# Kernel optimization log

Measured on AMD Instinct MI355X. Metric: run time of the kernel, lower is better.

The kernel has to match this reference:

```python
import jax, jax.numpy as jnp
import numpy as np

D_MODEL, H, D_K = 768, 12, 64
B, S = 2, 2048
NEG = -1.0e9


def setup_inputs() -> dict:
    key = jax.random.key(0)
    ks = jax.random.split(key, 7)
    q = jax.random.normal(ks[0], (B, S, D_MODEL), dtype=jnp.float32)
    k = jax.random.normal(ks[1], (B, S, D_MODEL), dtype=jnp.float32)
    v = jax.random.normal(ks[2], (B, S, D_MODEL), dtype=jnp.float32)
    mask = jnp.tril(jnp.ones((S, S), dtype=jnp.int32))[None, None]  # [1,1,S,S] causal
    sc = 1.0 / np.sqrt(D_MODEL)
    w_q = jax.random.normal(ks[3], (D_MODEL, D_MODEL), dtype=jnp.float32) * sc
    w_k = jax.random.normal(ks[4], (D_MODEL, D_MODEL), dtype=jnp.float32) * sc
    w_v = jax.random.normal(ks[5], (D_MODEL, D_MODEL), dtype=jnp.float32) * sc
    w_o = jax.random.normal(ks[6], (D_MODEL, D_MODEL), dtype=jnp.float32) * sc
    return {"q": q, "k": k, "v": v, "mask": mask,
            "w_q": w_q, "w_k": w_k, "w_v": w_v, "w_o": w_o}


def reference(q, k, v, mask, w_q, w_k, w_v, w_o):
    # nn.Linear(x) = x @ W.T ; split heads: [B,S,D] -> [B,H,S,Dk]
    def split_heads(x, w):
        y = jnp.einsum('bsd,ed->bse', x, w)
        return y.reshape(x.shape[0], x.shape[1], H, D_K).transpose(0, 2, 1, 3)

    qh = split_heads(q, w_q)
    kh = split_heads(k, w_k)
    vh = split_heads(v, w_v)
    scores = jnp.einsum('bhqd,bhkd->bhqk', qh, kh) / jnp.sqrt(jnp.float32(D_K))
    scores = jnp.where(mask == 0, jnp.float32(NEG), scores)
    attn = jax.nn.softmax(scores, axis=-1)  # dropout p=0 -> identity
    ctx = jnp.einsum('bhqk,bhkd->bhqd', attn, vh)
    ctx = ctx.transpose(0, 2, 1, 3).reshape(q.shape[0], q.shape[1], D_MODEL)
    return jnp.einsum('bsd,ed->bse', ctx, w_o)
```

## Files before the change

### kernel.cpp

```cpp
#include <hip/hip_runtime.h>

#define DM   768
#define HN   12
#define DKH  64
#define BSZ  2
#define SEQ  2048
#define MROWS (BSZ*SEQ)
#define NEGBIG -1.0e9f
#define NSLOT 40
#define QSCALE 0.18033688011112042f

typedef __bf16 bf16;
typedef __bf16 bf16x8 __attribute__((ext_vector_type(8)));
typedef __bf16 bf16x4 __attribute__((ext_vector_type(4)));
typedef float  f32x4  __attribute__((ext_vector_type(4)));
typedef unsigned int uint32;

__device__ __forceinline__ void gload_lds16(const void* g, void* l) {
    __builtin_amdgcn_global_load_lds(
        (const __attribute__((address_space(1))) char*)g,
        (__attribute__((address_space(3))) char*)l, 16, 0, 0);
}

__global__ __launch_bounds__(256) void gemm_qkv(
    const float* __restrict__ xq, const float* __restrict__ xk, const float* __restrict__ xv,
    const float* __restrict__ wq, const float* __restrict__ wk, const float* __restrict__ wv,
    bf16* __restrict__ qh, bf16* __restrict__ kh, bf16* __restrict__ vt)
{
    __shared__ float Asf[128 * 32];
    __shared__ float Bsf[128 * 32];

    const float* A; const float* Bw; bf16* Out; float qs;
    if      (blockIdx.z == 0) { A = xq; Bw = wq; Out = qh; qs = QSCALE; }
    else if (blockIdx.z == 1) { A = xk; Bw = wk; Out = kh; qs = 1.0f; }
    else                      { A = xv; Bw = wv; Out = vt; qs = 1.0f; }
    const bool vout = (blockIdx.z == 2);

    const int t = threadIdx.x, w = t >> 6, lane = t & 63;
    const int g = lane >> 4, lo = lane & 15;
    const int mt = blockIdx.x * 128, nt = blockIdx.y * 128;
    const int wr = (w >> 1) * 64, wc = (w & 1) * 64;

    f32x4 acc[4][4] = {};

    for (int k0 = 0; k0 < DM; k0 += 32) {
        #pragma unroll
        for (int i = 0; i < 4; i++) {
            int c = i * 256 + t;
            int row = c >> 3, cc = (c & 7) ^ (row & 7);
            gload_lds16(A  + (size_t)(mt + row) * DM + k0 + cc * 4, (char*)Asf + c * 16);
            gload_lds16(Bw + (size_t)(nt + row) * DM + k0 + cc * 4, (char*)Bsf + c * 16);
        }
        asm volatile("s_waitcnt vmcnt(0)" ::: "memory");
        __syncthreads();

        bf16x8 af[4], bfr[4];
        #pragma unroll
        for (int m = 0; m < 4; m++) {
            const char* rp = (const char*)Asf + (wr + m * 16 + lo) * 128;
            float4 f0 = *(const float4*)(rp + (((2 * g)     ^ (lo & 7)) << 4));
            float4 f1 = *(const float4*)(rp + (((2 * g + 1) ^ (lo & 7)) << 4));
            bf16x8 a;
            a[0] = (bf16)f0.x; a[1] = (bf16)f0.y; a[2] = (bf16)f0.z; a[3] = (bf16)f0.w;
            a[4] = (bf16)f1.x; a[5] = (bf16)f1.y; a[6] = (bf16)f1.z; a[7] = (bf16)f1.w;
            af[m] = a;
        }
        #pragma unroll
        for (int n = 0; n < 4; n++) {
            const char* rp = (const char*)Bsf + (wc + n * 16 + lo) * 128;
            float4 f0 = *(const float4*)(rp + (((2 * g)     ^ (lo & 7)) << 4));
            float4 f1 = *(const float4*)(rp + (((2 * g + 1) ^ (lo & 7)) << 4));
            bf16x8 b;
            b[0] = (bf16)f0.x; b[1] = (bf16)f0.y; b[2] = (bf16)f0.z; b[3] = (bf16)f0.w;
            b[4] = (bf16)f1.x; b[5] = (bf16)f1.y; b[6] = (bf16)f1.z; b[7] = (bf16)f1.w;
            bfr[n] = b;
        }
        #pragma unroll
        for (int m = 0; m < 4; m++)
            #pragma unroll
            for (int n = 0; n < 4; n++)
                acc[m][n] = __builtin_amdgcn_mfma_f32_16x16x32_bf16(af[m], bfr[n], acc[m][n], 0, 0, 0);
        __syncthreads();
    }

    if (!vout) {
        #pragma unroll
        for (int m = 0; m < 4; m++) {
            #pragma unroll
            for (int n = 0; n < 4; n++) {
                #pragma unroll
                for (int r = 0; r < 4; r++) {
                    int gm = mt + wr + m * 16 + g * 4 + r;
                    int gn = nt + wc + n * 16 + lo;
                    int b = gm >> 11, s = gm & 2047, h = gn >> 6, d = gn & 63;
                    Out[(((size_t)b * HN + h) * SEQ + s) * DKH + d] = (bf16)(acc[m][n][r] * qs);
                }
            }
        }
    } else {
        #pragma unroll
        for (int m = 0; m < 4; m++) {
            #pragma unroll
            for (int n = 0; n < 4; n++) {
                int gm = mt + wr + m * 16 + g * 4;
                int gn = nt + wc + n * 16 + lo;
                int b = gm >> 11, s0 = gm & 2047, h = gn >> 6, d = gn & 63;
                bf16x4 pk;
                #pragma unroll
                for (int r = 0; r < 4; r++) pk[r] = (bf16)acc[m][n][r];
                *(bf16x4*)&Out[(((size_t)b * HN + h) * DKH + d) * SEQ + s0] = pk;
            }
        }
    }
}

__global__ __launch_bounds__(256) void gemm_out(
    const bf16* __restrict__ Actx, const float* __restrict__ Bw, float* __restrict__ Out)
{
    __shared__ bf16  As[128 * 32];
    __shared__ float Bsf[128 * 32];

    const int t = threadIdx.x, w = t >> 6, lane = t & 63;
    const int g = lane >> 4, lo = lane & 15;
    const int mt = blockIdx.x * 128, nt = blockIdx.y * 128;
    const int wr = (w >> 1) * 64, wc = (w & 1) * 64;

    f32x4 acc[4][4] = {};

    for (int k0 = 0; k0 < DM; k0 += 32) {
        #pragma unroll
        for (int i = 0; i < 2; i++) {
            int c = i * 256 + t;
            int row = c >> 2, col = (c & 3) * 8;
            gload_lds16(Actx + (size_t)(mt + row) * DM + k0 + col, (char*)As + c * 16);
        }
        #pragma unroll
        for (int i = 0; i < 4; i++) {
            int c = i * 256 + t;
            int row = c >> 3, cc = (c & 7) ^ (row & 7);
            gload_lds16(Bw + (size_t)(nt + row) * DM + k0 + cc * 4, (char*)Bsf + c * 16);
        }
        asm volatile("s_waitcnt vmcnt(0)" ::: "memory");
        __syncthreads();

        bf16x8 af[4], bfr[4];
        #pragma unroll
        for (int m = 0; m < 4; m++)
            af[m] = *(const bf16x8*)&As[(wr + m * 16 + lo) * 32 + g * 8];
        #pragma unroll
        for (int n = 0; n < 4; n++) {
            const char* rp = (const char*)Bsf + (wc + n * 16 + lo) * 128;
            float4 f0 = *(const float4*)(rp + (((2 * g)     ^ (lo & 7)) << 4));
            float4 f1 = *(const float4*)(rp + (((2 * g + 1) ^ (lo & 7)) << 4));
            bf16x8 b;
            b[0] = (bf16)f0.x; b[1] = (bf16)f0.y; b[2] = (bf16)f0.z; b[3] = (bf16)f0.w;
            b[4] = (bf16)f1.x; b[5] = (bf16)f1.y; b[6] = (bf16)f1.z; b[7] = (bf16)f1.w;
            bfr[n] = b;
        }
        #pragma unroll
        for (int m = 0; m < 4; m++)
            #pragma unroll
            for (int n = 0; n < 4; n++)
                acc[m][n] = __builtin_amdgcn_mfma_f32_16x16x32_bf16(af[m], bfr[n], acc[m][n], 0, 0, 0);
        __syncthreads();
    }

    #pragma unroll
    for (int m = 0; m < 4; m++) {
        #pragma unroll
        for (int n = 0; n < 4; n++) {
            #pragma unroll
            for (int r = 0; r < 4; r++) {
                int gm = mt + wr + m * 16 + g * 4 + r;
                int gn = nt + wc + n * 16 + lo;
                Out[(size_t)gm * DM + gn] = acc[m][n][r];
            }
        }
    }
}

__global__ __launch_bounds__(256, 3) void flash_split(
    const bf16* __restrict__ qh, const bf16* __restrict__ kh,
    const bf16* __restrict__ vt, bf16* __restrict__ ctx,
    bf16* __restrict__ pO, float* __restrict__ pM, float* __restrict__ pL)
{
    __shared__ bf16 Ks[2][4096];
    __shared__ bf16 Vs[2][4096];
    __shared__ bf16 pl[4][1024];

    const int bid = blockIdx.x;
    const int slot = bid / 24;
    const int bh = bid % 24;

    int qt, p, np;
    if (slot < 16)      { qt = 15 - (slot >> 2); p = slot & 3;  np = 4; }
    else if (slot < 28) { int s = slot - 16; qt = 11 - s / 3; p = s % 3; np = 3; }
    else if (slot < 36) { int s = slot - 28; qt = 7 - (s >> 1); p = s & 1; np = 2; }
    else                { qt = 39 - slot; p = 0; np = 1; }

    const int T = 2 * qt + 2;
    const int bse = T / np, rem = T - bse * np;
    const int cnt   = bse + (p < rem ? 1 : 0);
    const int start = p * bse + (p < rem ? p : rem);

    const int qb = qt * 128;
    const int t = threadIdx.x, w = t >> 6, lane = t & 63;
    const int g = lane >> 4, lo = lane & 15;
    const size_t base = (size_t)bh * SEQ * DKH;
    const char* khead = (const char*)(kh + base);
    const char* vhead = (const char*)(vt + base);

    uint32 koff[2], voff[2];
    #pragma unroll
    for (int i = 0; i < 2; i++) {
        int c = w * 128 + i * 64 + lane;
        int r = c >> 3, s = c & 7;
        int sw = s ^ (r & 7);
        koff[i] = (uint32)(r * 128  + 16 * sw);
        voff[i] = (uint32)(r * 4096 + 16 * sw);
    }
    const uint32 kr0 = (uint32)(128 * lo + 16 * (g ^ (lo & 7)));
    const uint32 kr1 = kr0 ^ 64;

    uint32 pw[4], pr[2];
    #pragma unroll
    for (int cg = 0; cg < 4; cg++)
        pw[cg] = (uint32)(lo * 128 + (((2 * cg + (g >> 1)) ^ (lo & 7)) << 4) + (g & 1) * 8);
    #pragma unroll
    for (int kq = 0; kq < 2; kq++)
        pr[kq] = (uint32)(lo * 128 + (((4 * kq + g) ^ (lo & 7)) << 4));
    char* plb = (char*)&pl[w][0];

    const int qrow0 = qb + 16 * w + lo;
    const int qrow1 = qb + 64 + 16 * w + lo;
    const bf16* qp0 = qh + base + (size_t)qrow0 * DKH + g * 8;
    const bf16* qp1 = qh + base + (size_t)qrow1 * DKH + g * 8;
    bf16x8 qa0 = *(const bf16x8*)qp0;
    bf16x8 qa1 = *(const bf16x8*)(qp0 + 32);
    bf16x8 qb0 = *(const bf16x8*)qp1;
    bf16x8 qb1 = *(const bf16x8*)(qp1 + 32);

    f32x4 O0[4] = {}, O1[4] = {};
    float m0 = -1e30f, l0 = 0.0f, m1 = -1e30f, l1 = 0.0f;

    #pragma unroll
    for (int i = 0; i < 2; i++) {
        int c16 = (w * 128 + i * 64 + lane) * 16;
        gload_lds16(khead + (size_t)start * 8192 + koff[i], (char*)&Ks[0][0] + c16);
        gload_lds16(vhead + (size_t)start * 128  + voff[i], (char*)&Vs[0][0] + c16);
    }
    asm volatile("s_waitcnt vmcnt(0)" ::: "memory");
    __syncthreads();

    for (int it = 0; it < cnt; ++it) {
        const int kt = start + it;
        const int par = it & 1, nxt = par ^ 1;
        if (it + 1 < cnt) {
            const char* ks = khead + (size_t)(kt + 1) * 8192;
            const char* vs = vhead + (size_t)(kt + 1) * 128;
            #pragma unroll
            for (int i = 0; i < 2; i++) {
                int c16 = (w * 128 + i * 64 + lane) * 16;
                gload_lds16(ks + koff[i], (char*)&Ks[nxt][0] + c16);
                gload_lds16(vs + voff[i], (char*)&Vs[nxt][0] + c16);
            }
        }

        const bool act0  = (kt != T - 1);
        const bool diag0 = (kt == T - 2);
        const bool diag1 = (kt == T - 1);

        const char* Kp = (const char*)&Ks[par][0];
        f32x4 s0[4], s1[4];
        {
            bf16x8 kf0[4], kf1[4];
            #pragma unroll
            for (int cg = 0; cg < 4; cg++) {
                kf0[cg] = *(const bf16x8*)(Kp + cg * 2048 + kr0);
                kf1[cg] = *(const bf16x8*)(Kp + cg * 2048 + kr1);
            }
            __builtin_amdgcn_s_setprio(1);
            if (act0) {
                #pragma unroll
                for (int cg = 0; cg < 4; cg++) {
                    f32x4 z = {0.0f, 0.0f, 0.0f, 0.0f};
                    z = __builtin_amdgcn_mfma_f32_16x16x32_bf16(kf0[cg], qa0, z, 0, 0, 0);
                    z = __builtin_amdgcn_mfma_f32_16x16x32_bf16(kf1[cg], qa1, z, 0, 0, 0);
                    s0[cg] = z;
                }
            }
            #pragma unroll
            for (int cg = 0; cg < 4; cg++) {
                f32x4 z = {0.0f, 0.0f, 0.0f, 0.0f};
                z = __builtin_amdgcn_mfma_f32_16x16x32_bf16(kf0[cg], qb0, z, 0, 0, 0);
                z = __builtin_amdgcn_mfma_f32_16x16x32_bf16(kf1[cg], qb1, z, 0, 0, 0);
                s1[cg] = z;
            }
            __builtin_amdgcn_s_setprio(0);
        }

        if (act0 && diag0) {
            #pragma unroll
            for (int cg = 0; cg < 4; cg++)
                #pragma unroll
                for (int r = 0; r < 4; r++) {
                    int ki = kt * 64 + cg * 16 + 4 * g + r;
                    s0[cg][r] = (ki > qrow0) ? NEGBIG : s0[cg][r];
                }
        }
        if (diag1) {
            #pragma unroll
            for (int cg = 0; cg < 4; cg++)
                #pragma unroll
                for (int r = 0; r < 4; r++) {
                    int ki = kt * 64 + cg * 16 + 4 * g + r;
                    s1[cg][r] = (ki > qrow1) ? NEGBIG : s1[cg][r];
                }
        }

        if (act0) {
            float mx = fmaxf(fmaxf(fmaxf(s0[0][0], s0[0][1]), fmaxf(s0[0][2], s0[0][3])),
                             fmaxf(fmaxf(s0[1][0], s0[1][1]), fmaxf(s0[1][2], s0[1][3])));
            mx = fmaxf(mx, fmaxf(fmaxf(fmaxf(s0[2][0], s0[2][1]), fmaxf(s0[2][2], s0[2][3])),
                                 fmaxf(fmaxf(s0[3][0], s0[3][1]), fmaxf(s0[3][2], s0[3][3]))));
            mx = fmaxf(mx, __shfl_xor(mx, 16, 64));
            mx = fmaxf(mx, __shfl_xor(mx, 32, 64));
            if (!__all(mx - m0 <= 8.0f)) {
                float mnew = fmaxf(m0, mx);
                float scl = __builtin_exp2f(m0 - mnew);
                m0 = mnew; l0 *= scl;
                float s4[4];
                #pragma unroll
                for (int r = 0; r < 4; r++) s4[r] = __shfl(scl, 4 * g + r, 64);
                #pragma unroll
                for (int dg = 0; dg < 4; dg++)
                    #pragma unroll
                    for (int r = 0; r < 4; r++) O0[dg][r] *= s4[r];
            }
            float rs = 0.0f;
            #pragma unroll
            for (int cg = 0; cg < 4; cg++)
                #pragma unroll
                for (int r = 0; r < 4; r++) {
                    s0[cg][r] = __builtin_exp2f(s0[cg][r] - m0);
                    rs += s0[cg][r];
                }
            rs += __shfl_xor(rs, 16, 64);
            rs += __shfl_xor(rs, 32, 64);
            l0 += rs;
        }
        {
            float mx = fmaxf(fmaxf(fmaxf(s1[0][0], s1[0][1]), fmaxf(s1[0][2], s1[0][3])),
                             fmaxf(fmaxf(s1[1][0], s1[1][1]), fmaxf(s1[1][2], s1[1][3])));
            mx = fmaxf(mx, fmaxf(fmaxf(fmaxf(s1[2][0], s1[2][1]), fmaxf(s1[2][2], s1[2][3])),
                                 fmaxf(fmaxf(s1[3][0], s1[3][1]), fmaxf(s1[3][2], s1[3][3]))));
            mx = fmaxf(mx, __shfl_xor(mx, 16, 64));
            mx = fmaxf(mx, __shfl_xor(mx, 32, 64));
            if (!__all(mx - m1 <= 8.0f)) {
                float mnew = fmaxf(m1, mx);
                float scl = __builtin_exp2f(m1 - mnew);
                m1 = mnew; l1 *= scl;
                float s4[4];
                #pragma unroll
                for (int r = 0; r < 4; r++) s4[r] = __shfl(scl, 4 * g + r, 64);
                #pragma unroll
                for (int dg = 0; dg < 4; dg++)
                    #pragma unroll
                    for (int r = 0; r < 4; r++) O1[dg][r] *= s4[r];
            }
            float rs = 0.0f;
            #pragma unroll
            for (int cg = 0; cg < 4; cg++)
                #pragma unroll
                for (int r = 0; r < 4; r++) {
                    s1[cg][r] = __builtin_exp2f(s1[cg][r] - m1);
                    rs += s1[cg][r];
                }
            rs += __shfl_xor(rs, 16, 64);
            rs += __shfl_xor(rs, 32, 64);
            l1 += rs;
        }

        const char* Vp = (const char*)&Vs[par][0];
        bf16x8 vv[8];
        #pragma unroll
        for (int kq = 0; kq < 2; kq++)
            #pragma unroll
            for (int dblk = 0; dblk < 4; dblk++)
                vv[kq * 4 + dblk] = *(const bf16x8*)
                    (Vp + (dblk * 16 + lo) * 128 + 16 * ((4 * kq + g) ^ (lo & 7)));

        if (act0) {
            #pragma unroll
            for (int cg = 0; cg < 4; cg++) {
                bf16x4 pk;
                #pragma unroll
                for (int r = 0; r < 4; r++) pk[r] = (bf16)s0[cg][r];
                *(bf16x4*)(plb + pw[cg]) = pk;
            }
        }
        asm volatile("s_waitcnt lgkmcnt(0)" ::: "memory");
        __builtin_amdgcn_sched_barrier(0);
        if (act0) {
            __builtin_amdgcn_s_setprio(1);
            #pragma unroll
            for (int kq = 0; kq < 2; kq++) {
                bf16x8 pa = *(const bf16x8*)(plb + pr[kq]);
                #pragma unroll
                for (int dblk = 0; dblk < 4; dblk++)
                    O0[dblk] = __builtin_amdgcn_mfma_f32_16x16x32_bf16(pa, vv[kq * 4 + dblk], O0[dblk], 0, 0, 0);
            }
            __builtin_amdgcn_s_setprio(0);
        }
        __builtin_amdgcn_sched_barrier(0);
        {
            #pragma unroll
            for (int cg = 0; cg < 4; cg++) {
                bf16x4 pk;
                #pragma unroll
                for (int r = 0; r < 4; r++) pk[r] = (bf16)s1[cg][r];
                *(bf16x4*)(plb + pw[cg]) = pk;
            }
            asm volatile("s_waitcnt lgkmcnt(0)" ::: "memory");
            __builtin_amdgcn_sched_barrier(0);
            __builtin_amdgcn_s_setprio(1);
            #pragma unroll
            for (int kq = 0; kq < 2; kq++) {
                bf16x8 pa = *(const bf16x8*)(plb + pr[kq]);
                #pragma unroll
                for (int dblk = 0; dblk < 4; dblk++)
                    O1[dblk] = __builtin_amdgcn_mfma_f32_16x16x32_bf16(pa, vv[kq * 4 + dblk], O1[dblk], 0, 0, 0);
            }
            __builtin_amdgcn_s_setprio(0);
        }

        asm volatile("s_waitcnt vmcnt(0)" ::: "memory");
        __syncthreads();
    }

    if (np == 1) {
        const int b = bh / HN, h = bh % HN;
        float inv0[4], inv1[4];
        #pragma unroll
        for (int r = 0; r < 4; r++) {
            inv0[r] = 1.0f / __shfl(l0, 4 * g + r, 64);
            inv1[r] = 1.0f / __shfl(l1, 4 * g + r, 64);
        }
        #pragma unroll
        for (int dg = 0; dg < 4; dg++) {
            #pragma unroll
            for (int r = 0; r < 4; r++) {
                int row0 = qb + 16 * w + g * 4 + r;
                int row1 = qb + 64 + 16 * w + g * 4 + r;
                ctx[((size_t)(b * SEQ + row0)) * DM + h * DKH + dg * 16 + lo] =
                    (bf16)(O0[dg][r] * inv0[r]);
                ctx[((size_t)(b * SEQ + row1)) * DM + h * DKH + dg * 16 + lo] =
                    (bf16)(O1[dg][r] * inv1[r]);
            }
        }
    } else {
        const int pslot = bh * NSLOT + slot;
        bf16* po = pO + (size_t)pslot * 128 * 64;
        #pragma unroll
        for (int dg = 0; dg < 4; dg++) {
            #pragma unroll
            for (int r = 0; r < 4; r++) {
                int r0 = 16 * w + 4 * g + r;
                po[r0 * 64 + dg * 16 + lo]        = (bf16)O0[dg][r];
                po[(64 + r0) * 64 + dg * 16 + lo] = (bf16)O1[dg][r];
            }
        }
        if (g == 0) {
            pM[pslot * 128 + 16 * w + lo]      = m0;
            pL[pslot * 128 + 16 * w + lo]      = l0;
            pM[pslot * 128 + 64 + 16 * w + lo] = m1;
            pL[pslot * 128 + 64 + 16 * w + lo] = l1;
        }
    }
}

__global__ __launch_bounds__(256) void flash_combine(
    const bf16* __restrict__ pO, const float* __restrict__ pM,
    const float* __restrict__ pL, bf16* __restrict__ ctx)
{
    const int bh = blockIdx.x;
    const int qt = 4 + blockIdx.y;
    int np, s0;
    if (qt >= 12)     { np = 4; s0 = (15 - qt) * 4; }
    else if (qt >= 8) { np = 3; s0 = 16 + (11 - qt) * 3; }
    else              { np = 2; s0 = 28 + (7 - qt) * 2; }

    const int t = threadIdx.x;
    const int row = t >> 1, dh = (t & 1) * 32;
    const int pbase = bh * NSLOT + s0;

    float mi[4], wi[4];
    float mstar = -1e30f;
    #pragma unroll
    for (int i = 0; i < 4; i++)
        if (i < np) { mi[i] = pM[(pbase + i) * 128 + row]; mstar = fmaxf(mstar, mi[i]); }
    float lsum = 0.0f;
    #pragma unroll
    for (int i = 0; i < 4; i++)
        if (i < np) { wi[i] = __builtin_exp2f(mi[i] - mstar); lsum += wi[i] * pL[(pbase + i) * 128 + row]; }
    const float linv = 1.0f / lsum;

    const int b = bh / HN, h = bh % HN;
    bf16* crow = ctx + ((size_t)(b * SEQ + qt * 128 + row)) * DM + h * DKH + dh;

    #pragma unroll
    for (int d0 = 0; d0 < 32; d0 += 8) {
        float acc[8] = {};
        #pragma unroll
        for (int i = 0; i < 4; i++) {
            if (i < np) {
                bf16x8 o = *(const bf16x8*)&pO[((size_t)(pbase + i) * 128 + row) * 64 + dh + d0];
                #pragma unroll
                for (int j = 0; j < 8; j++) acc[j] += wi[i] * (float)o[j];
            }
        }
        bf16x8 ov;
        #pragma unroll
        for (int j = 0; j < 8; j++) ov[j] = (bf16)(acc[j] * linv);
        *(bf16x8*)(crow + d0) = ov;
    }
}

extern "C" void kernel_launch(void* const* d_in, const int* in_sizes, int n_in,
                              void* d_out, int out_size, void* d_ws, size_t ws_size,
                              hipStream_t stream) {
    const float* q  = (const float*)d_in[0];
    const float* k  = (const float*)d_in[1];
    const float* v  = (const float*)d_in[2];
    const float* wq = (const float*)d_in[4];
    const float* wk = (const float*)d_in[5];
    const float* wv = (const float*)d_in[6];
    const float* wo = (const float*)d_in[7];
    float* out = (float*)d_out;

    const size_t NX = (size_t)MROWS * DM;

    bf16* p = (bf16*)d_ws;
    bf16* qhp = p; p += NX;
    bf16* khp = p; p += NX;
    bf16* vtp = p; p += NX;
    bf16* ctxp = p; p += NX;
    bf16* pO = p; p += (size_t)24 * NSLOT * 128 * 64;
    float* pM = (float*)p;
    float* pL = pM + 24 * NSLOT * 128;

    gemm_qkv<<<dim3(MROWS / 128, DM / 128, 3), 256, 0, stream>>>(
        q, k, v, wq, wk, wv, qhp, khp, vtp);

    flash_split<<<24 * NSLOT, 256, 0, stream>>>(qhp, khp, vtp, ctxp, pO, pM, pL);
    flash_combine<<<dim3(24, 12), 256, 0, stream>>>(pO, pM, pL, ctxp);

    gemm_out<<<dim3(MROWS / 128, DM / 128), 256, 0, stream>>>(ctxp, wo, out);
}
```

Measured before the change: 116.3 us.

## Pre-convert QKV inputs to bf16 and double-buffer QKV GEMM; split P buffers in attention

Adds a conversion kernel that turns the fp32 activations and Q/K/V weights into bf16 in workspace. The QKV GEMM then loads bf16 tiles with BK=64 into double-buffered LDS, prefetching the next tile while computing the current one, so the per-tile fp32-to-bf16 conversion in the inner loop goes away. In flash_split, the P tiles for both row groups get separate LDS halves, which lets both be written right after softmax and both PV MFMA groups run back-to-back without an intermediate wait. The cost is an extra kernel launch plus a full read and write of the fp32 inputs, more LDS per block, and reuse of the bf16 input buffers as the split-partial workspace.

```diff
diff --git a/kernel.cpp b/kernel.cpp
--- a/kernel.cpp
+++ b/kernel.cpp
@@ -22,15 +22,39 @@
         (__attribute__((address_space(3))) char*)l, 16, 0, 0);
 }
 
+__global__ __launch_bounds__(256) void cvt6(
+    const float* __restrict__ a, const float* __restrict__ b, const float* __restrict__ c,
+    const float* __restrict__ d3, const float* __restrict__ e, const float* __restrict__ f,
+    bf16* __restrict__ x, bf16* __restrict__ y, bf16* __restrict__ z,
+    bf16* __restrict__ u, bf16* __restrict__ v, bf16* __restrict__ wbuf,
+    int nx, int nw)
+{
+    const float* s; bf16* d; int n;
+    switch (blockIdx.y) {
+        case 0: s = a;  d = x;    n = nx; break;
+        case 1: s = b;  d = y;    n = nx; break;
+        case 2: s = c;  d = z;    n = nx; break;
+        case 3: s = d3; d = u;    n = nw; break;
+        case 4: s = e;  d = v;    n = nw; break;
+        default: s = f; d = wbuf; n = nw; break;
+    }
+    int i = (blockIdx.x * 256 + threadIdx.x) * 4;
+    if (i + 3 < n) {
+        float4 vv = *(const float4*)(s + i);
+        bf16x4 o; o[0] = (bf16)vv.x; o[1] = (bf16)vv.y; o[2] = (bf16)vv.z; o[3] = (bf16)vv.w;
+        *(bf16x4*)(d + i) = o;
+    }
+}
+
 __global__ __launch_bounds__(256) void gemm_qkv(
-    const float* __restrict__ xq, const float* __restrict__ xk, const float* __restrict__ xv,
-    const float* __restrict__ wq, const float* __restrict__ wk, const float* __restrict__ wv,
+    const bf16* __restrict__ xq, const bf16* __restrict__ xk, const bf16* __restrict__ xv,
+    const bf16* __restrict__ wq, const bf16* __restrict__ wk, const bf16* __restrict__ wv,
     bf16* __restrict__ qh, bf16* __restrict__ kh, bf16* __restrict__ vt)
 {
-    __shared__ float Asf[128 * 32];
-    __shared__ float Bsf[128 * 32];
-
-    const float* A; const float* Bw; bf16* Out; float qs;
+    __shared__ bf16 As[2][128 * 64];
+    __shared__ bf16 Bs[2][128 * 64];
+
+    const bf16* A; const bf16* Bw; bf16* Out; float qs;
     if      (blockIdx.z == 0) { A = xq; Bw = wq; Out = qh; qs = QSCALE; }
     else if (blockIdx.z == 1) { A = xk; Bw = wk; Out = kh; qs = 1.0f; }
     else                      { A = xv; Bw = wv; Out = vt; qs = 1.0f; }
@@ -42,13 +66,118 @@
     const int wr = (w >> 1) * 64, wc = (w & 1) * 64;
 
     f32x4 acc[4][4] = {};
+    const int NT = DM / 64;
+
+    uint32 soff[4];
+    #pragma unroll
+    for (int i = 0; i < 4; i++) {
+        int c = i * 256 + t;
+        int row = c >> 3, s = c & 7;
+        soff[i] = (uint32)(row * DM + (s ^ (row & 7)) * 8);
+    }
+
+    #pragma unroll
+    for (int i = 0; i < 4; i++) {
+        int c16 = (i * 256 + t) * 16;
+        gload_lds16(A  + (size_t)mt * DM + soff[i], (char*)&As[0][0] + c16);
+        gload_lds16(Bw + (size_t)nt * DM + soff[i], (char*)&Bs[0][0] + c16);
+    }
+    asm volatile("s_waitcnt vmcnt(0)" ::: "memory");
+    __syncthreads();
+
+    for (int it = 0; it < NT; ++it) {
+        const int par = it & 1, nxt = par ^ 1;
+        if (it + 1 < NT) {
+            const size_t k0 = (size_t)(it + 1) * 64;
+            #pragma unroll
+            for (int i = 0; i < 4; i++) {
+                int c16 = (i * 256 + t) * 16;
+                gload_lds16(A  + (size_t)mt * DM + k0 + soff[i], (char*)&As[nxt][0] + c16);
+                gload_lds16(Bw + (size_t)nt * DM + k0 + soff[i], (char*)&Bs[nxt][0] + c16);
+            }
+        }
+
+        const char* Ap = (const char*)&As[par][0];
+        const char* Bp = (const char*)&Bs[par][0];
+        #pragma unroll
+        for (int h = 0; h < 2; h++) {
+            bf16x8 af[4], bfr[4];
+            #pragma unroll
+            for (int m = 0; m < 4; m++) {
+                int row = wr + m * 16 + lo;
+                af[m] = *(const bf16x8*)(Ap + row * 128 + 16 * ((4 * h + g) ^ (lo & 7)));
+            }
+            #pragma unroll
+            for (int n = 0; n < 4; n++) {
+                int row = wc + n * 16 + lo;
+                bfr[n] = *(const bf16x8*)(Bp + row * 128 + 16 * ((4 * h + g) ^ (lo & 7)));
+            }
+            #pragma unroll
+            for (int m = 0; m < 4; m++)
+                #pragma unroll
+                for (int n = 0; n < 4; n++)
+                    acc[m][n] = __builtin_amdgcn_mfma_f32_16x16x32_bf16(af[m], bfr[n], acc[m][n], 0, 0, 0);
+        }
+
+        asm volatile("s_waitcnt vmcnt(0)" ::: "memory");
+        __syncthreads();
+    }
+
+    if (!vout) {
+        #pragma unroll
+        for (int m = 0; m < 4; m++) {
+            #pragma unroll
+            for (int n = 0; n < 4; n++) {
+                #pragma unroll
+                for (int r = 0; r < 4; r++) {
+                    int gm = mt + wr + m * 16 + g * 4 + r;
+                    int gn = nt + wc + n * 16 + lo;
+                    int b = gm >> 11, s = gm & 2047, h = gn >> 6, d = gn & 63;
+                    Out[(((size_t)b * HN + h) * SEQ + s) * DKH + d] = (bf16)(acc[m][n][r] * qs);
+                }
+            }
+        }
+    } else {
+        #pragma unroll
+        for (int m = 0; m < 4; m++) {
+            #pragma unroll
+            for (int n = 0; n < 4; n++) {
+                int gm = mt + wr + m * 16 + g * 4;
+                int gn = nt + wc + n * 16 + lo;
+                int b = gm >> 11, s0 = gm & 2047, h = gn >> 6, d = gn & 63;
+                bf16x4 pk;
+                #pragma unroll
+                for (int r = 0; r < 4; r++) pk[r] = (bf16)acc[m][n][r];
+                *(bf16x4*)&Out[(((size_t)b * HN + h) * DKH + d) * SEQ + s0] = pk;
+            }
+        }
+    }
+}
+
+__global__ __launch_bounds__(256) void gemm_out(
+    const bf16* __restrict__ Actx, const float* __restrict__ Bw, float* __restrict__ Out)
+{
+    __shared__ bf16  As[128 * 32];
+    __shared__ float Bsf[128 * 32];
+
+    const int t = threadIdx.x, w = t >> 6, lane = t & 63;
+    const int g = lane >> 4, lo = lane & 15;
+    const int mt = blockIdx.x * 128, nt = blockIdx.y * 128;
+    const int wr = (w >> 1) * 64, wc = (w & 1) * 64;
+
+    f32x4 acc[4][4] = {};
 
     for (int k0 = 0; k0 < DM; k0 += 32) {
+        #pragma unroll
+        for (int i = 0; i < 2; i++) {
+            int c = i * 256 + t;
+            int row = c >> 2, col = (c & 3) * 8;
+            gload_lds16(Actx + (size_t)(mt + row) * DM + k0 + col, (char*)As + c * 16);
+        }
         #pragma unroll
         for (int i = 0; i < 4; i++) {
             int c = i * 256 + t;
             int row = c >> 3, cc = (c & 7) ^ (row & 7);
-            gload_lds16(A  + (size_t)(mt + row) * DM + k0 + cc * 4, (char*)Asf + c * 16);
             gload_lds16(Bw + (size_t)(nt + row) * DM + k0 + cc * 4, (char*)Bsf + c * 16);
         }
         asm volatile("s_waitcnt vmcnt(0)" ::: "memory");
@@ -56,15 +185,8 @@
 
         bf16x8 af[4], bfr[4];
         #pragma unroll
-        for (int m = 0; m < 4; m++) {
-            const char* rp = (const char*)Asf + (wr + m * 16 + lo) * 128;
-            float4 f0 = *(const float4*)(rp + (((2 * g)     ^ (lo & 7)) << 4));
-            float4 f1 = *(const float4*)(rp + (((2 * g + 1) ^ (lo & 7)) << 4));
-            bf16x8 a;
-            a[0] = (bf16)f0.x; a[1] = (bf16)f0.y; a[2] = (bf16)f0.z; a[3] = (bf16)f0.w;
-            a[4] = (bf16)f1.x; a[5] = (bf16)f1.y; a[6] = (bf16)f1.z; a[7] = (bf16)f1.w;
-            af[m] = a;
-        }
+        for (int m = 0; m < 4; m++)
+            af[m] = *(const bf16x8*)&As[(wr + m * 16 + lo) * 32 + g * 8];
         #pragma unroll
         for (int n = 0; n < 4; n++) {
             const char* rp = (const char*)Bsf + (wc + n * 16 + lo) * 128;
@@ -83,88 +205,6 @@
         __syncthreads();
     }
 
-    if (!vout) {
-        #pragma unroll
-        for (int m = 0; m < 4; m++) {
-            #pragma unroll
-            for (int n = 0; n < 4; n++) {
-                #pragma unroll
-                for (int r = 0; r < 4; r++) {
-                    int gm = mt + wr + m * 16 + g * 4 + r;
-                    int gn = nt + wc + n * 16 + lo;
-                    int b = gm >> 11, s = gm & 2047, h = gn >> 6, d = gn & 63;
-                    Out[(((size_t)b * HN + h) * SEQ + s) * DKH + d] = (bf16)(acc[m][n][r] * qs);
-                }
-            }
-        }
-    } else {
-        #pragma unroll
-        for (int m = 0; m < 4; m++) {
-            #pragma unroll
-            for (int n = 0; n < 4; n++) {
-                int gm = mt + wr + m * 16 + g * 4;
-                int gn = nt + wc + n * 16 + lo;
-                int b = gm >> 11, s0 = gm & 2047, h = gn >> 6, d = gn & 63;
-                bf16x4 pk;
-                #pragma unroll
-                for (int r = 0; r < 4; r++) pk[r] = (bf16)acc[m][n][r];
-                *(bf16x4*)&Out[(((size_t)b * HN + h) * DKH + d) * SEQ + s0] = pk;
-            }
-        }
-    }
-}
-
-__global__ __launch_bounds__(256) void gemm_out(
-    const bf16* __restrict__ Actx, const float* __restrict__ Bw, float* __restrict__ Out)
-{
-    __shared__ bf16  As[128 * 32];
-    __shared__ float Bsf[128 * 32];
-
-    const int t = threadIdx.x, w = t >> 6, lane = t & 63;
-    const int g = lane >> 4, lo = lane & 15;
-    const int mt = blockIdx.x * 128, nt = blockIdx.y * 128;
-    const int wr = (w >> 1) * 64, wc = (w & 1) * 64;
-
-    f32x4 acc[4][4] = {};
-
-    for (int k0 = 0; k0 < DM; k0 += 32) {
-        #pragma unroll
-        for (int i = 0; i < 2; i++) {
-            int c = i * 256 + t;
-            int row = c >> 2, col = (c & 3) * 8;
-            gload_lds16(Actx + (size_t)(mt + row) * DM + k0 + col, (char*)As + c * 16);
-        }
-        #pragma unroll
-        for (int i = 0; i < 4; i++) {
-            int c = i * 256 + t;
-            int row = c >> 3, cc = (c & 7) ^ (row & 7);
-            gload_lds16(Bw + (size_t)(nt + row) * DM + k0 + cc * 4, (char*)Bsf + c * 16);
-        }
-        asm volatile("s_waitcnt vmcnt(0)" ::: "memory");
-        __syncthreads();
-
-        bf16x8 af[4], bfr[4];
-        #pragma unroll
-        for (int m = 0; m < 4; m++)
-            af[m] = *(const bf16x8*)&As[(wr + m * 16 + lo) * 32 + g * 8];
-        #pragma unroll
-        for (int n = 0; n < 4; n++) {
-            const char* rp = (const char*)Bsf + (wc + n * 16 + lo) * 128;
-            float4 f0 = *(const float4*)(rp + (((2 * g)     ^ (lo & 7)) << 4));
-            float4 f1 = *(const float4*)(rp + (((2 * g + 1) ^ (lo & 7)) << 4));
-            bf16x8 b;
-            b[0] = (bf16)f0.x; b[1] = (bf16)f0.y; b[2] = (bf16)f0.z; b[3] = (bf16)f0.w;
-            b[4] = (bf16)f1.x; b[5] = (bf16)f1.y; b[6] = (bf16)f1.z; b[7] = (bf16)f1.w;
-            bfr[n] = b;
-        }
-        #pragma unroll
-        for (int m = 0; m < 4; m++)
-            #pragma unroll
-            for (int n = 0; n < 4; n++)
-                acc[m][n] = __builtin_amdgcn_mfma_f32_16x16x32_bf16(af[m], bfr[n], acc[m][n], 0, 0, 0);
-        __syncthreads();
-    }
-
     #pragma unroll
     for (int m = 0; m < 4; m++) {
         #pragma unroll
@@ -186,7 +226,7 @@
 {
     __shared__ bf16 Ks[2][4096];
     __shared__ bf16 Vs[2][4096];
-    __shared__ bf16 pl[4][1024];
+    __shared__ bf16 pl[4][2048];
 
     const int bid = blockIdx.x;
     const int slot = bid / 24;
@@ -348,6 +388,13 @@
             rs += __shfl_xor(rs, 16, 64);
             rs += __shfl_xor(rs, 32, 64);
             l0 += rs;
+            #pragma unroll
+            for (int cg = 0; cg < 4; cg++) {
+                bf16x4 pk;
+                #pragma unroll
+                for (int r = 0; r < 4; r++) pk[r] = (bf16)s0[cg][r];
+                *(bf16x4*)(plb + pw[cg]) = pk;
+            }
         }
         {
             float mx = fmaxf(fmaxf(fmaxf(s1[0][0], s1[0][1]), fmaxf(s1[0][2], s1[0][3])),
@@ -379,6 +426,13 @@
             rs += __shfl_xor(rs, 16, 64);
             rs += __shfl_xor(rs, 32, 64);
             l1 += rs;
+            #pragma unroll
+            for (int cg = 0; cg < 4; cg++) {
+                bf16x4 pk;
+                #pragma unroll
+                for (int r = 0; r < 4; r++) pk[r] = (bf16)s1[cg][r];
+                *(bf16x4*)(plb + 2048 + pw[cg]) = pk;
+            }
         }
 
         const char* Vp = (const char*)&Vs[par][0];
@@ -389,20 +443,11 @@
             for (int dblk = 0; dblk < 4; dblk++)
                 vv[kq * 4 + dblk] = *(const bf16x8*)
                     (Vp + (dblk * 16 + lo) * 128 + 16 * ((4 * kq + g) ^ (lo & 7)));
-
-        if (act0) {
-            #pragma unroll
-            for (int cg = 0; cg < 4; cg++) {
-                bf16x4 pk;
-                #pragma unroll
-                for (int r = 0; r < 4; r++) pk[r] = (bf16)s0[cg][r];
-                *(bf16x4*)(plb + pw[cg]) = pk;
-            }
-        }
         asm volatile("s_waitcnt lgkmcnt(0)" ::: "memory");
         __builtin_amdgcn_sched_barrier(0);
+
+        __builtin_amdgcn_s_setprio(1);
         if (act0) {
-            __builtin_amdgcn_s_setprio(1);
             #pragma unroll
             for (int kq = 0; kq < 2; kq++) {
                 bf16x8 pa = *(const bf16x8*)(plb + pr[kq]);
@@ -410,29 +455,15 @@
                 for (int dblk = 0; dblk < 4; dblk++)
                     O0[dblk] = __builtin_amdgcn_mfma_f32_16x16x32_bf16(pa, vv[kq * 4 + dblk], O0[dblk], 0, 0, 0);
             }
-            __builtin_amdgcn_s_setprio(0);
-        }
-        __builtin_amdgcn_sched_barrier(0);
-        {
-            #pragma unroll
-            for (int cg = 0; cg < 4; cg++) {
-                bf16x4 pk;
-                #pragma unroll
-                for (int r = 0; r < 4; r++) pk[r] = (bf16)s1[cg][r];
-                *(bf16x4*)(plb + pw[cg]) = pk;
-            }
-            asm volatile("s_waitcnt lgkmcnt(0)" ::: "memory");
-            __builtin_amdgcn_sched_barrier(0);
-            __builtin_amdgcn_s_setprio(1);
-            #pragma unroll
-            for (int kq = 0; kq < 2; kq++) {
-                bf16x8 pa = *(const bf16x8*)(plb + pr[kq]);
-                #pragma unroll
-                for (int dblk = 0; dblk < 4; dblk++)
-                    O1[dblk] = __builtin_amdgcn_mfma_f32_16x16x32_bf16(pa, vv[kq * 4 + dblk], O1[dblk], 0, 0, 0);
-            }
-            __builtin_amdgcn_s_setprio(0);
-        }
+        }
+        #pragma unroll
+        for (int kq = 0; kq < 2; kq++) {
+            bf16x8 pa = *(const bf16x8*)(plb + 2048 + pr[kq]);
+            #pragma unroll
+            for (int dblk = 0; dblk < 4; dblk++)
+                O1[dblk] = __builtin_amdgcn_mfma_f32_16x16x32_bf16(pa, vv[kq * 4 + dblk], O1[dblk], 0, 0, 0);
+        }
+        __builtin_amdgcn_s_setprio(0);
 
         asm volatile("s_waitcnt vmcnt(0)" ::: "memory");
         __syncthreads();
@@ -539,18 +570,30 @@
     float* out = (float*)d_out;
 
     const size_t NX = (size_t)MROWS * DM;
+    const size_t NW = (size_t)DM * DM;
 
     bf16* p = (bf16*)d_ws;
+    bf16* xq  = p; p += NX;
+    bf16* xk  = p; p += NX;
+    bf16* xv  = p; p += NX;
+    bf16* wqb = p; p += NW;
+    bf16* wkb = p; p += NW;
+    bf16* wvb = p; p += NW;
     bf16* qhp = p; p += NX;
     bf16* khp = p; p += NX;
     bf16* vtp = p; p += NX;
     bf16* ctxp = p; p += NX;
-    bf16* pO = p; p += (size_t)24 * NSLOT * 128 * 64;
-    float* pM = (float*)p;
+
+    bf16*  pO = xq;
+    float* pM = (float*)(xq + (size_t)24 * NSLOT * 128 * 64);
     float* pL = pM + 24 * NSLOT * 128;
 
+    cvt6<<<dim3(NX / 1024, 6), 256, 0, stream>>>(q, k, v, wq, wk, wv,
+                                                 xq, xk, xv, wqb, wkb, wvb,
+                                                 (int)NX, (int)NW);
+
     gemm_qkv<<<dim3(MROWS / 128, DM / 128, 3), 256, 0, stream>>>(
-        q, k, v, wq, wk, wv, qhp, khp, vtp);
+        xq, xk, xv, wqb, wkb, wvb, qhp, khp, vtp);
 
     flash_split<<<24 * NSLOT, 256, 0, stream>>>(qhp, khp, vtp, ctxp, pO, pM, pL);
     flash_combine<<<dim3(24, 12), 256, 0, stream>>>(pO, pM, pL, ctxp);
```

Measured after the change: 118.4 us. About the same (+1.8%).
